# Kernel optimization log

Measured on AMD Instinct MI355X. Metric: run time of the kernel, lower is better.

Reference implementation:

```python
import jax, jax.numpy as jnp
import numpy as np

B, S, D = 2, 2048, 1024
H, DQK, DV = 16, 64, 64
DECAY = 0.85


def _fractal_weights(seq_len: int, decay: float) -> np.ndarray:
    # Dragon-curve hierarchical weights: earlier (coarser) positions get higher
    # weight; weight decays by `decay` per hierarchy level. Normalized to sum 1,
    # matching DragonCurveGenerator.get_hierarchical_weights semantics.
    idx = np.arange(seq_len)
    level = np.floor(np.log2(idx + 1)).astype(np.int32)
    w = decay ** level.astype(np.float32)
    return (w / w.sum()).astype(np.float32)


def setup_inputs() -> dict:
    key = jax.random.key(0)
    kx, kq, kk, kv, ko = jax.random.split(key, 5)
    s = 1.0 / np.sqrt(D)
    return {
        "x": jax.random.normal(kx, (B, S, D), dtype=jnp.float32),
        "Wq": jax.random.normal(kq, (D, H * DQK), dtype=jnp.float32) * s,
        "Wk": jax.random.normal(kk, (D, H * DQK), dtype=jnp.float32) * s,
        "Wv": jax.random.normal(kv, (D, H * DV), dtype=jnp.float32) * s,
        "Wo": jax.random.normal(ko, (H * DV, D), dtype=jnp.float32) * s,
        "fractal_weights": jnp.asarray(_fractal_weights(S, DECAY)),
    }


def reference(x, Wq, Wk, Wv, Wo, fractal_weights):
    b, s, _ = x.shape
    # Projections (Linear with bias=False); weights stored as (in, out).
    Q = (x @ Wq).reshape(b, s, H, DQK).transpose(0, 2, 1, 3)  # [B,H,S,Dqk]
    K = (x @ Wk).reshape(b, s, H, DQK).transpose(0, 2, 1, 3)
    V = (x @ Wv).reshape(b, s, H, DV).transpose(0, 2, 1, 3)   # [B,H,S,Dv]
    scale = 1.0 / jnp.sqrt(jnp.asarray(DQK, dtype=x.dtype))
    scores = jnp.einsum("bhqd,bhkd->bhqk", Q, K) * scale      # [B,H,S,S]
    # Multiplicative per-key fractal bias applied BEFORE softmax.
    scores = scores * fractal_weights[None, None, None, :]
    attn = jax.nn.softmax(scores, axis=-1)
    out = jnp.einsum("bhqk,bhkd->bhqd", attn, V)               # [B,H,S,Dv]
    out = out.transpose(0, 2, 1, 3).reshape(b, s, H * DV)
    return out @ Wo                                            # [B,S,D]
```

## Files before the change

kernel.cpp:

```cpp
#include <hip/hip_runtime.h>
#include <hip/hip_bf16.h>
#include <stdint.h>

#define B_  2
#define S_  2048
#define D_  1024
#define H_  16
#define DH_ 64

typedef __attribute__((ext_vector_type(8))) __bf16    bf16x8;
typedef __attribute__((ext_vector_type(8))) _Float16  f16x8;
typedef __attribute__((ext_vector_type(4))) _Float16  f16x4;
typedef __attribute__((ext_vector_type(2))) __fp16    fp16x2;
typedef __attribute__((ext_vector_type(4))) float     f32x4;

__device__ inline unsigned short f2bf(float f) {
    union { float f; uint32_t u; } v; v.f = f;
    uint32_t r = (v.u + 0x7fffu + ((v.u >> 16) & 1u)) >> 16;
    return (unsigned short)r;
}

__device__ __forceinline__ void g2l16(const unsigned short* g, unsigned short* l) {
    __builtin_amdgcn_global_load_lds(
        (const __attribute__((address_space(1))) unsigned int*)g,
        (__attribute__((address_space(3))) unsigned int*)l,
        16, 0, 0);
}


__global__ void convert_x(const float* __restrict__ x, unsigned short* __restrict__ xb, int n) {
    int i = (blockIdx.x * blockDim.x + threadIdx.x) * 4;
    if (i < n) {
        float4 v = *(const float4*)(x + i);
        ushort4 o;
        o.x = f2bf(v.x); o.y = f2bf(v.y); o.z = f2bf(v.z); o.w = f2bf(v.w);
        *(ushort4*)(xb + i) = o;
    }
}

__global__ void transpose_w(const float* __restrict__ s0, const float* __restrict__ s1,
                            const float* __restrict__ s2, const float* __restrict__ s3,
                            unsigned short* __restrict__ d0, unsigned short* __restrict__ d1,
                            unsigned short* __restrict__ d2, unsigned short* __restrict__ d3) {
    __shared__ float tile[32][33];
    const float* src; unsigned short* dst;
    switch (blockIdx.z) {
        case 0: src = s0; dst = d0; break;
        case 1: src = s1; dst = d1; break;
        case 2: src = s2; dst = d2; break;
        default: src = s3; dst = d3; break;
    }
    int n0 = blockIdx.x * 32, k0 = blockIdx.y * 32;
    int tx = threadIdx.x, ty = threadIdx.y;
    for (int j = 0; j < 32; j += 8)
        tile[ty + j][tx] = src[(long)(k0 + ty + j) * 1024 + n0 + tx];
    __syncthreads();
    for (int j = 0; j < 32; j += 8)
        dst[(long)(n0 + ty + j) * 1024 + k0 + tx] = f2bf(tile[tx][ty + j]);
}

template<int MODE>
__global__ __launch_bounds__(256, 2)
void gemm128(const unsigned short* __restrict__ A, const unsigned short* __restrict__ Bt,
             unsigned short* __restrict__ Qo, unsigned short* __restrict__ Ko,
             unsigned short* __restrict__ Vt, float* __restrict__ Cout)
{
    __shared__ __align__(16) unsigned short As[128 * 64];
    __shared__ __align__(16) unsigned short Bs[128 * 64];
    const int tid  = threadIdx.x;
    const int lane = tid & 63, wid = tid >> 6;
    const int quad = lane >> 4, l15 = lane & 15;
    const int wm = wid >> 1, wn = wid & 1;
    const int bm = blockIdx.y, bn = blockIdx.x;
    const int K = 1024;
    f32x4 acc[4][4] = {};
    const long Abase = (long)bm * 128 * K;
    const long Bbase = (long)bn * 128 * K;

    for (int k0 = 0; k0 < K; k0 += 64) {
        __syncthreads();
#pragma unroll
        for (int i = 0; i < 4; i++) {
            int slot = i * 256 + wid * 64 + lane;
            int row = slot >> 3, cp = slot & 7;
            int c = cp ^ (row & 7);
            g2l16(A + Abase + (long)row * K + k0 + c * 8, &As[(i * 256 + wid * 64) * 8]);
        }
#pragma unroll
        for (int i = 0; i < 4; i++) {
            int slot = i * 256 + wid * 64 + lane;
            int row = slot >> 3, cp = slot & 7;
            int c = cp ^ (row & 7);
            g2l16(Bt + Bbase + (long)row * K + k0 + c * 8, &Bs[(i * 256 + wid * 64) * 8]);
        }
        __syncthreads();
#pragma unroll
        for (int ks = 0; ks < 2; ks++) {
            bf16x8 af[4], bfr[4];
#pragma unroll
            for (int t = 0; t < 4; t++) {
                int ra = wm * 64 + t * 16 + l15;
                af[t]  = *(const bf16x8*)(As + ra * 64 + (((ks * 4 + quad) ^ (l15 & 7))) * 8);
                int rb = wn * 64 + t * 16 + l15;
                bfr[t] = *(const bf16x8*)(Bs + rb * 64 + (((ks * 4 + quad) ^ (l15 & 7))) * 8);
            }
#pragma unroll
            for (int tm = 0; tm < 4; tm++)
#pragma unroll
                for (int tn = 0; tn < 4; tn++)
                    acc[tm][tn] = __builtin_amdgcn_mfma_f32_16x16x32_bf16(af[tm], bfr[tn], acc[tm][tn], 0, 0, 0);
        }
    }

    const float Cq = 0.125f * 1.44269504f;
    for (int tm = 0; tm < 4; tm++)
        for (int tn = 0; tn < 4; tn++)
            for (int r = 0; r < 4; r++) {
                int gm = bm * 128 + wm * 64 + tm * 16 + quad * 4 + r;
                int gn = bn * 128 + wn * 64 + tn * 16 + l15;
                float v = acc[tm][tn][r];
                if (MODE == 0) {
                    int b = gm >> 11, s = gm & 2047;
                    if (gn < 1024) {
                        int h = gn >> 6, d = gn & 63;
                        Qo[(((long)(b * H_ + h) * S_ + s) << 6) + d] = f2bf(v * Cq);
                    } else if (gn < 2048) {
                        int g = gn - 1024; int h = g >> 6, d = g & 63;
                        Ko[(((long)(b * H_ + h) * S_ + s) << 6) + d] = f2bf(v);
                    } else {
                        int g = gn - 2048; int h = g >> 6, d = g & 63;
                        union { _Float16 h; unsigned short u; } cv;
                        cv.h = (_Float16)v;
                        Vt[((long)(b * H_ + h) * DH_ + d) * S_ + s] = cv.u;
                    }
                } else {
                    Cout[(long)gm * 1024 + gn] = v;
                }
            }
}

__global__ __launch_bounds__(256, 2)
void attn_kernel(const unsigned short* __restrict__ Q, const unsigned short* __restrict__ Kb,
                 const unsigned short* __restrict__ Vt, const float* __restrict__ fw,
                 unsigned short* __restrict__ O)
{
    __shared__ __align__(16) unsigned short Ks[2][64 * 64];
    __shared__ __align__(16) unsigned short Vs[2][64 * 64];

    const int tid  = threadIdx.x;
    const int lane = tid & 63, wid = tid >> 6;
    const int quad = lane >> 4, l15 = lane & 15;
    const int bh = blockIdx.y;
    const int qt = blockIdx.x;

    const unsigned short* Kg = Kb + (long)bh * S_ * DH_;
    const unsigned short* Vg = Vt + (long)bh * (long)DH_ * S_;

    bf16x8 qf[2][2];
#pragma unroll
    for (int s = 0; s < 2; s++) {
        const unsigned short* Qp = Q + ((long)bh * S_ + qt * 128 + wid * 32 + s * 16 + l15) * DH_ + quad * 8;
        qf[s][0] = *(const bf16x8*)(Qp);
        qf[s][1] = *(const bf16x8*)(Qp + 32);
    }

    auto issue = [&](int buf, int kt) {
#pragma unroll
        for (int i = 0; i < 2; i++) {
            int slot = wid * 128 + i * 64 + lane;
            int row = slot >> 3, cp = slot & 7;
            int c = cp ^ (row & 7);
            g2l16(Kg + ((long)(kt * 64 + row) * 64 + c * 8), &Ks[buf][(wid * 128 + i * 64) * 8]);
        }
#pragma unroll
        for (int i = 0; i < 2; i++) {
            int slot = wid * 128 + i * 64 + lane;
            int row = slot >> 3, cp = slot & 7;
            int c = cp ^ (row & 7);
            g2l16(Vg + ((long)row * S_ + kt * 64 + c * 8), &Vs[buf][(wid * 128 + i * 64) * 8]);
        }
    };

    f32x4 oacc[2][4] = {};
    float l_r[2] = {0.f, 0.f};

    issue(0, 0);
    __syncthreads();

    for (int kt = 0; kt < S_ / 64; kt++) {
        const int cur = kt & 1;
        if (kt + 1 < S_ / 64) issue(1 - cur, kt + 1);

        f32x4 wvc[4];
#pragma unroll
        for (int kc = 0; kc < 4; kc++) {
            float4 w = *(const float4*)(fw + kt * 64 + kc * 16 + quad * 4);
            wvc[kc][0] = w.x; wvc[kc][1] = w.y; wvc[kc][2] = w.z; wvc[kc][3] = w.w;
        }

        const unsigned short* Kc = &Ks[cur][0];
        const unsigned short* Vc = &Vs[cur][0];

        f32x4 sacc[2][4] = {};
#pragma unroll
        for (int kc = 0; kc < 4; kc++) {
            int row = kc * 16 + l15;
            bf16x8 k0 = *(const bf16x8*)(Kc + (row * 8 + (quad       ^ (l15 & 7))) * 8);
            bf16x8 k1 = *(const bf16x8*)(Kc + (row * 8 + ((4 + quad) ^ (l15 & 7))) * 8);
#pragma unroll
            for (int s = 0; s < 2; s++) {
                sacc[s][kc] = __builtin_amdgcn_mfma_f32_16x16x32_bf16(k0, qf[s][0], sacc[s][kc], 0, 0, 0);
                sacc[s][kc] = __builtin_amdgcn_mfma_f32_16x16x32_bf16(k1, qf[s][1], sacc[s][kc], 0, 0, 0);
            }
        }

        f16x4 pk[2][4];
#pragma unroll
        for (int s = 0; s < 2; s++)
#pragma unroll
            for (int kc = 0; kc < 4; kc++) {
                float p0 = __builtin_amdgcn_exp2f(sacc[s][kc][0] * wvc[kc][0]);
                float p1 = __builtin_amdgcn_exp2f(sacc[s][kc][1] * wvc[kc][1]);
                float p2 = __builtin_amdgcn_exp2f(sacc[s][kc][2] * wvc[kc][2]);
                float p3 = __builtin_amdgcn_exp2f(sacc[s][kc][3] * wvc[kc][3]);
                l_r[s] += (p0 + p1) + (p2 + p3);
                union { fp16x2 h; unsigned int u; } a, b;
                a.h = __builtin_amdgcn_cvt_pkrtz(p0, p1);
                b.h = __builtin_amdgcn_cvt_pkrtz(p2, p3);
                union { uint2 u; f16x4 v; } pku;
                pku.u = make_uint2(a.u, b.u);
                pk[s][kc] = pku.v;
            }

#pragma unroll
        for (int kc = 0; kc < 4; kc++)
#pragma unroll
            for (int dt = 0; dt < 4; dt++) {
                int row = dt * 16 + l15;
                int pos = (kc * 2 + (quad >> 1)) ^ (l15 & 7);
                f16x4 vf = *(const f16x4*)(Vc + row * 64 + pos * 8 + (quad & 1) * 4);
                oacc[0][dt] = __builtin_amdgcn_mfma_f32_16x16x16f16(pk[0][kc], vf, oacc[0][dt], 0, 0, 0);
                oacc[1][dt] = __builtin_amdgcn_mfma_f32_16x16x16f16(pk[1][kc], vf, oacc[1][dt], 0, 0, 0);
            }

        __syncthreads();
    }

#pragma unroll
    for (int s = 0; s < 2; s++) {
        l_r[s] += __shfl_xor(l_r[s], 16);
        l_r[s] += __shfl_xor(l_r[s], 32);
    }

    int b = bh >> 4, h = bh & 15;
#pragma unroll
    for (int s = 0; s < 2; s++)
#pragma unroll
        for (int r = 0; r < 4; r++) {
            float inv = 1.0f / __shfl(l_r[s], quad * 4 + r);
            int srow = qt * 128 + wid * 32 + s * 16 + quad * 4 + r;
#pragma unroll
            for (int dt = 0; dt < 4; dt++)
                O[((long)(b * S_ + srow)) * 1024 + h * DH_ + dt * 16 + l15] = f2bf(oacc[s][dt][r] * inv);
        }
}


extern "C" void kernel_launch(void* const* d_in, const int* in_sizes, int n_in,
                              void* d_out, int out_size, void* d_ws, size_t ws_size,
                              hipStream_t stream)
{
    const float* x  = (const float*)d_in[0];
    const float* Wq = (const float*)d_in[1];
    const float* Wk = (const float*)d_in[2];
    const float* Wv = (const float*)d_in[3];
    const float* Wo = (const float*)d_in[4];
    const float* fw = (const float*)d_in[5];
    float* out = (float*)d_out;

    char* ws = (char*)d_ws;
    unsigned short* xb    = (unsigned short*)(ws);
    unsigned short* WqkvT = (unsigned short*)(ws + 8388608);
    unsigned short* WoT   = (unsigned short*)(ws + 14680064);
    unsigned short* Qb    = (unsigned short*)(ws + 16777216);
    unsigned short* Kb    = (unsigned short*)(ws + 25165824);
    unsigned short* Vt    = (unsigned short*)(ws + 33554432);
    unsigned short* Ob    = xb;

    convert_x<<<dim3((B_ * S_ * D_) / 4 / 256), dim3(256), 0, stream>>>(x, xb, B_ * S_ * D_);
    transpose_w<<<dim3(32, 32, 4), dim3(32, 8), 0, stream>>>(
        Wq, Wk, Wv, Wo,
        WqkvT, WqkvT + 1024 * 1024, WqkvT + 2 * 1024 * 1024, WoT);
    gemm128<0><<<dim3(24, 32), dim3(256), 0, stream>>>(xb, WqkvT, Qb, Kb, Vt, (float*)nullptr);
    attn_kernel<<<dim3(S_ / 128, B_ * H_), dim3(256), 0, stream>>>(Qb, Kb, Vt, fw, Ob);
    gemm128<1><<<dim3(8, 32), dim3(256), 0, stream>>>(Ob, WoT,
        (unsigned short*)nullptr, (unsigned short*)nullptr, (unsigned short*)nullptr, out);
}
```

Measured before the change: 212.5 us.

## Fold fractal key weights into K projection and shrink attention blocks

Scales K by the per-key fractal weight in the QKV GEMM epilogue. This removes the per-tile weight loads and multiplies from the attention inner loop. Attention blocks also shrink from 256 to 128 threads covering 64 query rows, so there are twice as many blocks, for better occupancy and load balance. The trade-off is that each K/V tile is reused by fewer queries, so K/V traffic into LDS doubles, and K rounds to bf16 after the weight scaling.

```diff
diff --git a/kernel.cpp b/kernel.cpp
--- a/kernel.cpp
+++ b/kernel.cpp
@@ -63,7 +63,8 @@
 __global__ __launch_bounds__(256, 2)
 void gemm128(const unsigned short* __restrict__ A, const unsigned short* __restrict__ Bt,
              unsigned short* __restrict__ Qo, unsigned short* __restrict__ Ko,
-             unsigned short* __restrict__ Vt, float* __restrict__ Cout)
+             unsigned short* __restrict__ Vt, float* __restrict__ Cout,
+             const float* __restrict__ fw)
 {
     __shared__ __align__(16) unsigned short As[128 * 64];
     __shared__ __align__(16) unsigned short Bs[128 * 64];
@@ -126,7 +127,7 @@
                         Qo[(((long)(b * H_ + h) * S_ + s) << 6) + d] = f2bf(v * Cq);
                     } else if (gn < 2048) {
                         int g = gn - 1024; int h = g >> 6, d = g & 63;
-                        Ko[(((long)(b * H_ + h) * S_ + s) << 6) + d] = f2bf(v);
+                        Ko[(((long)(b * H_ + h) * S_ + s) << 6) + d] = f2bf(v * fw[s]);
                     } else {
                         int g = gn - 2048; int h = g >> 6, d = g & 63;
                         union { _Float16 h; unsigned short u; } cv;
@@ -139,9 +140,9 @@
             }
 }
 
-__global__ __launch_bounds__(256, 2)
+__global__ __launch_bounds__(128, 2)
 void attn_kernel(const unsigned short* __restrict__ Q, const unsigned short* __restrict__ Kb,
-                 const unsigned short* __restrict__ Vt, const float* __restrict__ fw,
+                 const unsigned short* __restrict__ Vt,
                  unsigned short* __restrict__ O)
 {
     __shared__ __align__(16) unsigned short Ks[2][64 * 64];
@@ -159,25 +160,27 @@
     bf16x8 qf[2][2];
 #pragma unroll
     for (int s = 0; s < 2; s++) {
-        const unsigned short* Qp = Q + ((long)bh * S_ + qt * 128 + wid * 32 + s * 16 + l15) * DH_ + quad * 8;
+        const unsigned short* Qp = Q + ((long)bh * S_ + qt * 64 + wid * 32 + s * 16 + l15) * DH_ + quad * 8;
         qf[s][0] = *(const bf16x8*)(Qp);
         qf[s][1] = *(const bf16x8*)(Qp + 32);
     }
 
     auto issue = [&](int buf, int kt) {
 #pragma unroll
-        for (int i = 0; i < 2; i++) {
-            int slot = wid * 128 + i * 64 + lane;
-            int row = slot >> 3, cp = slot & 7;
-            int c = cp ^ (row & 7);
-            g2l16(Kg + ((long)(kt * 64 + row) * 64 + c * 8), &Ks[buf][(wid * 128 + i * 64) * 8]);
-        }
-#pragma unroll
-        for (int i = 0; i < 2; i++) {
-            int slot = wid * 128 + i * 64 + lane;
-            int row = slot >> 3, cp = slot & 7;
-            int c = cp ^ (row & 7);
-            g2l16(Vg + ((long)row * S_ + kt * 64 + c * 8), &Vs[buf][(wid * 128 + i * 64) * 8]);
+        for (int i = 0; i < 4; i++) {
+            int base = i * 128 + wid * 64;
+            int slot = base + lane;
+            int row = slot >> 3, cp = slot & 7;
+            int c = cp ^ (row & 7);
+            g2l16(Kg + ((long)(kt * 64 + row) * 64 + c * 8), &Ks[buf][base * 8]);
+        }
+#pragma unroll
+        for (int i = 0; i < 4; i++) {
+            int base = i * 128 + wid * 64;
+            int slot = base + lane;
+            int row = slot >> 3, cp = slot & 7;
+            int c = cp ^ (row & 7);
+            g2l16(Vg + ((long)row * S_ + kt * 64 + c * 8), &Vs[buf][base * 8]);
         }
     };
 
@@ -190,13 +193,6 @@
     for (int kt = 0; kt < S_ / 64; kt++) {
         const int cur = kt & 1;
         if (kt + 1 < S_ / 64) issue(1 - cur, kt + 1);
-
-        f32x4 wvc[4];
-#pragma unroll
-        for (int kc = 0; kc < 4; kc++) {
-            float4 w = *(const float4*)(fw + kt * 64 + kc * 16 + quad * 4);
-            wvc[kc][0] = w.x; wvc[kc][1] = w.y; wvc[kc][2] = w.z; wvc[kc][3] = w.w;
-        }
 
         const unsigned short* Kc = &Ks[cur][0];
         const unsigned short* Vc = &Vs[cur][0];
@@ -219,10 +215,10 @@
         for (int s = 0; s < 2; s++)
 #pragma unroll
             for (int kc = 0; kc < 4; kc++) {
-                float p0 = __builtin_amdgcn_exp2f(sacc[s][kc][0] * wvc[kc][0]);
-                float p1 = __builtin_amdgcn_exp2f(sacc[s][kc][1] * wvc[kc][1]);
-                float p2 = __builtin_amdgcn_exp2f(sacc[s][kc][2] * wvc[kc][2]);
-                float p3 = __builtin_amdgcn_exp2f(sacc[s][kc][3] * wvc[kc][3]);
+                float p0 = __builtin_amdgcn_exp2f(sacc[s][kc][0]);
+                float p1 = __builtin_amdgcn_exp2f(sacc[s][kc][1]);
+                float p2 = __builtin_amdgcn_exp2f(sacc[s][kc][2]);
+                float p3 = __builtin_amdgcn_exp2f(sacc[s][kc][3]);
                 l_r[s] += (p0 + p1) + (p2 + p3);
                 union { fp16x2 h; unsigned int u; } a, b;
                 a.h = __builtin_amdgcn_cvt_pkrtz(p0, p1);
@@ -258,7 +254,7 @@
 #pragma unroll
         for (int r = 0; r < 4; r++) {
             float inv = 1.0f / __shfl(l_r[s], quad * 4 + r);
-            int srow = qt * 128 + wid * 32 + s * 16 + quad * 4 + r;
+            int srow = qt * 64 + wid * 32 + s * 16 + quad * 4 + r;
 #pragma unroll
             for (int dt = 0; dt < 4; dt++)
                 O[((long)(b * S_ + srow)) * 1024 + h * DH_ + dt * 16 + l15] = f2bf(oacc[s][dt][r] * inv);
@@ -291,8 +287,8 @@
     transpose_w<<<dim3(32, 32, 4), dim3(32, 8), 0, stream>>>(
         Wq, Wk, Wv, Wo,
         WqkvT, WqkvT + 1024 * 1024, WqkvT + 2 * 1024 * 1024, WoT);
-    gemm128<0><<<dim3(24, 32), dim3(256), 0, stream>>>(xb, WqkvT, Qb, Kb, Vt, (float*)nullptr);
-    attn_kernel<<<dim3(S_ / 128, B_ * H_), dim3(256), 0, stream>>>(Qb, Kb, Vt, fw, Ob);
+    gemm128<0><<<dim3(24, 32), dim3(256), 0, stream>>>(xb, WqkvT, Qb, Kb, Vt, (float*)nullptr, fw);
+    attn_kernel<<<dim3(S_ / 64, B_ * H_), dim3(128), 0, stream>>>(Qb, Kb, Vt, Ob);
     gemm128<1><<<dim3(8, 32), dim3(256), 0, stream>>>(Ob, WoT,
-        (unsigned short*)nullptr, (unsigned short*)nullptr, (unsigned short*)nullptr, out);
-}
+        (unsigned short*)nullptr, (unsigned short*)nullptr, (unsigned short*)nullptr, out, (const float*)nullptr);
+}
```

Measured after the change: 200.5 us. 5.6% less time.
